# Optimization experiments

Measured on AMD Instinct MI355X. Metric: run time of the kernel, lower is better.

## Reference

```python
import jax, jax.numpy as jnp
import numpy as np

V, D, C, L, F = 32000, 1024, 2048, 6, 4096
B, S = 2, 2048


def _layer_norm(x, w, b, eps=1e-5):
    mu = jnp.mean(x, axis=-1, keepdims=True)
    var = jnp.mean(jnp.square(x - mu), axis=-1, keepdims=True)
    return (x - mu) * jax.lax.rsqrt(var + eps) * w + b


def setup_inputs() -> dict:
    key = jax.random.key(0)
    ks = jax.random.split(key, 16)
    s = 0.02
    inp = {
        "tokens": jax.random.randint(ks[0], (B, S), 0, V),
        "embed_table": jax.random.normal(ks[1], (V, D), jnp.float32) * s,
        "pos_table": jax.random.normal(ks[2], (C, D), jnp.float32) * s,
        # stacked per-layer params [L, ...]
        "ln1_w": jnp.ones((L, D), jnp.float32),
        "ln1_b": jnp.zeros((L, D), jnp.float32),
        "qkv_w": jax.random.normal(ks[3], (L, 3 * D, D), jnp.float32) * s,
        "qkv_b": jnp.zeros((L, 3 * D), jnp.float32),
        "ln2_w": jnp.ones((L, D), jnp.float32),
        "ln2_b": jnp.zeros((L, D), jnp.float32),
        "ffa_w": jax.random.normal(ks[4], (L, F, D), jnp.float32) * s,
        "ffa_b": jnp.zeros((L, F), jnp.float32),
        "ffb_w": jax.random.normal(ks[5], (L, D, F), jnp.float32) * s,
        "ffb_b": jnp.zeros((L, D), jnp.float32),
        "out_w": jax.random.normal(ks[6], (V, D), jnp.float32) * s,
    }
    return inp


def _forward(tokens, embed_table, pos_table, ln1_w, ln1_b, qkv_w, qkv_b,
             ln2_w, ln2_b, ffa_w, ffa_b, ffb_w, ffb_b, out_w):
    Sx = tokens.shape[1]
    h = embed_table[tokens] + pos_table[:Sx][None, :, :]  # [B,S,D]
    causal = jnp.triu(jnp.ones((Sx, Sx), bool), k=1)       # True = masked
    scale = jnp.float32(D) ** 0.5

    def block(h, p):
        l1w, l1b, qw, qb, l2w, l2b, aw, ab, bw, bb = p
        a = _layer_norm(h, l1w, l1b)
        qkv = jnp.einsum('bsd,ed->bse', a, qw) + qb       # [B,S,3D]
        q, k, v = jnp.split(qkv, 3, axis=-1)
        scores = jnp.einsum('bsd,btd->bst', q, k)          # [B,S,S]
        scores = jnp.where(causal[None], -jnp.inf, scores)
        attn = jax.nn.softmax(scores / scale, axis=-1)
        h = h + jnp.einsum('bst,btd->bsd', attn, v)
        f = _layer_norm(h, l2w, l2b)
        f = jax.nn.relu(jnp.einsum('bsd,fd->bsf', f, aw) + ab)
        h = h + jnp.einsum('bsf,df->bsd', f, bw) + bb
        return h, None

    params = (ln1_w, ln1_b, qkv_w, qkv_b, ln2_w, ln2_b, ffa_w, ffa_b, ffb_w, ffb_b)
    h, _ = jax.lax.scan(block, h, params)
    # OutputLayer applies only the Linear (output_norm is defined but unused)
    return jnp.einsum('bsd,vd->bsv', h, out_w)


def reference(tokens, embed_table, pos_table, ln1_w, ln1_b, qkv_w, qkv_b,
              ln2_w, ln2_b, ffa_w, ffa_b, ffb_w, ffb_b, out_w):
    return _forward(tokens, embed_table, pos_table, ln1_w, ln1_b, qkv_w, qkv_b,
                    ln2_w, ln2_b, ffa_w, ffa_b, ffb_w, ffb_b, out_w)
```

## Files before the change

kernel.cpp:

```cpp
#include <hip/hip_runtime.h>

#define Dm 1024
#define Sm 2048
#define Bm 2
#define Lm 6
#define Fm 4096
#define Vm 32000
#define MT (Bm*Sm)

typedef unsigned short u16;
typedef unsigned int   u32;
typedef __attribute__((ext_vector_type(8))) short bf16x8;
typedef __attribute__((ext_vector_type(4))) float f32x4;

__device__ __forceinline__ u16 f2bf(float f) {
  u32 u = __float_as_uint(f);
  u += 0x7fffu + ((u >> 16) & 1u);
  return (u16)(u >> 16);
}
__device__ __forceinline__ u32 pack2(float a, float b) {
  return (u32)f2bf(a) | ((u32)f2bf(b) << 16);
}
__device__ __forceinline__ void gload16(const void* g, void* l) {
  __builtin_amdgcn_global_load_lds(
      (const __attribute__((address_space(1))) void*)g,
      (__attribute__((address_space(3))) void*)l, 16, 0, 0);
}

__global__ __launch_bounds__(256) void embed_kernel(
    const int* __restrict__ tok, const float* __restrict__ emb,
    const float* __restrict__ pos, float* __restrict__ h)
{
  int i  = blockIdx.x * 256 + threadIdx.x;
  int d  = (i & (Dm/4 - 1)) * 4;
  int bs = i >> 8;
  int s  = bs & (Sm - 1);
  int t  = tok[bs];
  float4 e = *(const float4*)(emb + (size_t)t * Dm + d);
  float4 p = *(const float4*)(pos + (size_t)s * Dm + d);
  float4 r; r.x = e.x + p.x; r.y = e.y + p.y; r.z = e.z + p.z; r.w = e.w + p.w;
  *(float4*)(h + (size_t)bs * Dm + d) = r;
}

__global__ __launch_bounds__(256) void ln_kernel(
    const float* __restrict__ x, const float* __restrict__ w,
    const float* __restrict__ b, u16* __restrict__ o)
{
  __shared__ float red[8];
  int row = blockIdx.x, tid = threadIdx.x;
  const float* xr = x + (size_t)row * Dm;
  float4 v = *(const float4*)(xr + tid * 4);
  float s1 = v.x + v.y + v.z + v.w;
  float s2 = v.x*v.x + v.y*v.y + v.z*v.z + v.w*v.w;
  #pragma unroll
  for (int off = 32; off; off >>= 1) {
    s1 += __shfl_down(s1, off, 64);
    s2 += __shfl_down(s2, off, 64);
  }
  int lane = tid & 63, wv = tid >> 6;
  if (!lane) { red[wv] = s1; red[4 + wv] = s2; }
  __syncthreads();
  s1 = red[0] + red[1] + red[2] + red[3];
  s2 = red[4] + red[5] + red[6] + red[7];
  float mu = s1 * (1.f / Dm);
  float rs = rsqrtf(s2 * (1.f / Dm) - mu * mu + 1e-5f);
  float4 wv4 = *(const float4*)(w + tid * 4);
  float4 bv4 = *(const float4*)(b + tid * 4);
  uint2 pk;
  pk.x = pack2((v.x - mu) * rs * wv4.x + bv4.x, (v.y - mu) * rs * wv4.y + bv4.y);
  pk.y = pack2((v.z - mu) * rs * wv4.z + bv4.z, (v.w - mu) * rs * wv4.w + bv4.w);
  *(uint2*)(o + (size_t)row * Dm + tid * 4) = pk;
}

__global__ __launch_bounds__(256) void softmax_kernel(
    const float* __restrict__ sc, u16* __restrict__ at)
{
  __shared__ float red[8];
  int gr = blockIdx.x;
  int s  = gr & (Sm - 1);
  const float* x = sc + (size_t)gr * Sm;
  u16* o = at + (size_t)gr * Sm;
  int tid = threadIdx.x;
  float4 v0 = *(const float4*)(x + tid * 8);
  float4 v1 = *(const float4*)(x + tid * 8 + 4);
  float vals[8] = {v0.x, v0.y, v0.z, v0.w, v1.x, v1.y, v1.z, v1.w};
  float mx = -1e30f;
  #pragma unroll
  for (int j = 0; j < 8; ++j) {
    int t = tid * 8 + j;
    vals[j] = (t <= s) ? vals[j] * 0.03125f : -1e30f;
    mx = fmaxf(mx, vals[j]);
  }
  #pragma unroll
  for (int off = 32; off; off >>= 1) mx = fmaxf(mx, __shfl_down(mx, off, 64));
  int lane = tid & 63, wv = tid >> 6;
  if (!lane) red[wv] = mx;
  __syncthreads();
  mx = fmaxf(fmaxf(red[0], red[1]), fmaxf(red[2], red[3]));
  __syncthreads();
  float e[8], sm = 0.f;
  #pragma unroll
  for (int j = 0; j < 8; ++j) {
    int t = tid * 8 + j;
    e[j] = (t <= s) ? __expf(vals[j] - mx) : 0.f;
    sm += e[j];
  }
  #pragma unroll
  for (int off = 32; off; off >>= 1) sm += __shfl_down(sm, off, 64);
  if (!lane) red[wv] = sm;
  __syncthreads();
  sm = red[0] + red[1] + red[2] + red[3];
  float inv = 1.f / sm;
  uint4 p;
  p.x = pack2(e[0]*inv, e[1]*inv); p.y = pack2(e[2]*inv, e[3]*inv);
  p.z = pack2(e[4]*inv, e[5]*inv); p.w = pack2(e[6]*inv, e[7]*inv);
  *(uint4*)(o + tid * 8) = p;
}

__global__ __launch_bounds__(256) void cvt8_kernel(
    const float* __restrict__ x, u16* __restrict__ o)
{
  size_t i = ((size_t)blockIdx.x * 256 + threadIdx.x) * 8;
  float4 v0 = *(const float4*)(x + i);
  float4 v1 = *(const float4*)(x + i + 4);
  uint4 p; p.x = pack2(v0.x, v0.y); p.y = pack2(v0.z, v0.w);
  p.z = pack2(v1.x, v1.y); p.w = pack2(v1.z, v1.w);
  *(uint4*)(o + i) = p;
}

__global__ __launch_bounds__(256) void cvtw_kernel(
    const float* __restrict__ qw, const float* __restrict__ aw,
    const float* __restrict__ bw, u16* __restrict__ o)
{
  int b = blockIdx.x;
  const float* src; u16* dst; int idx;
  if (b < 1536)      { src = qw; dst = o;                     idx = b; }
  else if (b < 3584) { src = aw; dst = o + 3*Dm*Dm;           idx = b - 1536; }
  else               { src = bw; dst = o + 3*Dm*Dm + Fm*Dm;   idx = b - 3584; }
  size_t i = ((size_t)idx * 256 + threadIdx.x) * 8;
  float4 v0 = *(const float4*)(src + i);
  float4 v1 = *(const float4*)(src + i + 4);
  uint4 p; p.x = pack2(v0.x, v0.y); p.y = pack2(v0.z, v0.w);
  p.z = pack2(v1.x, v1.y); p.w = pack2(v1.z, v1.w);
  *(uint4*)(dst + i) = p;
}

__global__ __launch_bounds__(256) void vtr_kernel(
    const u16* __restrict__ v, u16* __restrict__ vT)
{
  __shared__ u16 t[64][64];
  int b = blockIdx.z;
  int s0 = blockIdx.x * 64, d0 = blockIdx.y * 64;
  const u16* src = v + ((size_t)b * Sm + s0) * (3 * Dm) + d0;
  int tid = threadIdx.x;
  int rr = tid >> 3, cc = (tid & 7) * 8;
  #pragma unroll
  for (int it = 0; it < 2; ++it) {
    int r = rr + it * 32;
    uint4 x = *(const uint4*)(src + (size_t)r * (3 * Dm) + cc);
    *(uint4*)&t[r][cc ^ (((r >> 3) & 7) << 3)] = x;
  }
  __syncthreads();
  u16* dst = vT + ((size_t)b * Dm + d0) * Sm + s0;
  #pragma unroll
  for (int it = 0; it < 2; ++it) {
    int d = rr + it * 32;
    u16 tmp[8];
    #pragma unroll
    for (int j = 0; j < 8; ++j) {
      int r = cc + j;
      tmp[j] = t[r][d ^ (((r >> 3) & 7) << 3)];
    }
    *(uint4*)(dst + (size_t)d * Sm + cc) = *(uint4*)tmp;
  }
}

enum { EPI_F32 = 0, EPI_BF16 = 1, EPI_RELU_BF16 = 2, EPI_RES = 3 };

__global__ __launch_bounds__(256, 2)
void gemm_kernel(const u16* __restrict__ A, const u16* __restrict__ B,
                 float* __restrict__ outF, u16* __restrict__ outB,
                 const float* __restrict__ bias, const float* __restrict__ resid,
                 int N, int K, int lda, int ldb,
                 long sA, long sB, long sO, long sR,
                 int mshift, int epi, int swz)
{
  __shared__ __align__(16) short As[128 * 64];
  __shared__ __align__(16) short Bs[128 * 64];

  const int z = blockIdx.z;
  int bid = blockIdx.x;
  if (swz) { int cpx = gridDim.x >> 3; bid = (bid & 7) * cpx + (bid >> 3); }
  const int m0 = (bid & ((1 << mshift) - 1)) << 7;
  const int n0 = (bid >> mshift) << 7;

  const u16* Az = A + (size_t)z * sA;
  const u16* Bz = B + (size_t)z * sB;

  const int tid = threadIdx.x;
  const int l   = tid & 63;
  const int w   = tid >> 6;
  const int sub = l >> 3;
  const int colb = ((l & 7) ^ sub) << 4;
  const int row0 = w * 32 + sub;

  const char* gA = (const char*)(Az + (size_t)(m0 + row0) * lda) + colb;
  const char* gB = (const char*)(Bz + (size_t)(n0 + row0) * ldb) + colb;
  const size_t stepA = (size_t)8 * lda * 2;
  const size_t stepB = (size_t)8 * ldb * 2;
  char* lA = (char*)As + w * 4096;
  char* lB = (char*)Bs + w * 4096;

  const int wm   = (w >> 1) * 64;
  const int wn   = (w & 1) * 64;
  const int lrow = l & 15;
  const int kgrp = l >> 4;

  f32x4 acc[4][4];
  #pragma unroll
  for (int i = 0; i < 4; ++i)
    #pragma unroll
    for (int j = 0; j < 4; ++j)
      acc[i][j] = (f32x4){0.f, 0.f, 0.f, 0.f};

  for (int k0 = 0; k0 < K; k0 += 64) {
    __syncthreads();
    const char* ga = gA + (size_t)k0 * 2;
    const char* gb = gB + (size_t)k0 * 2;
    #pragma unroll
    for (int c = 0; c < 4; ++c) {
      gload16(ga + c * stepA, lA + c * 1024);
      gload16(gb + c * stepB, lB + c * 1024);
    }
    __syncthreads();
    #pragma unroll
    for (int kk = 0; kk < 2; ++kk) {
      bf16x8 af[4], bf_[4];
      #pragma unroll
      for (int i = 0; i < 4; ++i) {
        int ar = wm + i * 16 + lrow;
        af[i]  = *(const bf16x8*)((const char*)As + ar * 128 +
                                  ((kk * 64 + kgrp * 16) ^ ((ar & 7) << 4)));
        int br = wn + i * 16 + lrow;
        bf_[i] = *(const bf16x8*)((const char*)Bs + br * 128 +
                                  ((kk * 64 + kgrp * 16) ^ ((br & 7) << 4)));
      }
      #pragma unroll
      for (int i = 0; i < 4; ++i)
        #pragma unroll
        for (int j = 0; j < 4; ++j)
          acc[i][j] = __builtin_amdgcn_mfma_f32_16x16x32_bf16(af[i], bf_[j], acc[i][j], 0, 0, 0);
    }
  }

  #pragma unroll
  for (int i = 0; i < 4; ++i) {
    #pragma unroll
    for (int j = 0; j < 4; ++j) {
      #pragma unroll
      for (int r = 0; r < 4; ++r) {
        int m = m0 + wm + i * 16 + kgrp * 4 + r;
        int n = n0 + wn + j * 16 + lrow;
        float v = acc[i][j][r];
        if (bias) v += bias[n];
        if (epi == EPI_F32) {
          outF[(size_t)z * sO + (size_t)m * N + n] = v;
        } else if (epi == EPI_BF16) {
          outB[(size_t)m * N + n] = f2bf(v);
        } else if (epi == EPI_RELU_BF16) {
          outB[(size_t)m * N + n] = f2bf(fmaxf(v, 0.f));
        } else {
          float* o = outF + (size_t)z * sO;
          const float* rsd = resid + (size_t)z * sR;
          o[(size_t)m * N + n] = rsd[(size_t)m * N + n] + v;
        }
      }
    }
  }
}

extern "C" void kernel_launch(void* const* d_in, const int* in_sizes, int n_in,
                              void* d_out, int out_size, void* d_ws, size_t ws_size,
                              hipStream_t stream)
{
  const int*   tok  = (const int*)d_in[0];
  const float* emb  = (const float*)d_in[1];
  const float* pos  = (const float*)d_in[2];
  const float* ln1w = (const float*)d_in[3];
  const float* ln1b = (const float*)d_in[4];
  const float* qkvw = (const float*)d_in[5];
  const float* qkvb = (const float*)d_in[6];
  const float* ln2w = (const float*)d_in[7];
  const float* ln2b = (const float*)d_in[8];
  const float* ffaw = (const float*)d_in[9];
  const float* ffab = (const float*)d_in[10];
  const float* ffbw = (const float*)d_in[11];
  const float* ffbb = (const float*)d_in[12];
  const float* outw = (const float*)d_in[13];
  float* out = (float*)d_out;

  char* p = (char*)d_ws;
  float* h      = (float*)p;  p += (size_t)MT * Dm * 4;
  u16*   a      = (u16*)p;    p += (size_t)MT * Dm * 2;
  u16*   hb     = (u16*)p;    p += (size_t)MT * Dm * 2;
  u16*   qkv    = (u16*)p;    p += (size_t)MT * 3 * Dm * 2;
  u16*   vT     = (u16*)p;    p += (size_t)Bm * Dm * Sm * 2;
  float* scores = (float*)p;  p += (size_t)Bm * Sm * Sm * 4;
  u16*   attn   = (u16*)p;    p += (size_t)Bm * Sm * Sm * 2;
  u16*   f      = (u16*)p;    p += (size_t)MT * Fm * 2;
  u16*   wlb    = (u16*)p;    p += (size_t)(3*Dm*Dm + Fm*Dm + Dm*Fm) * 2;
  u16*   owb    = qkv;

  embed_kernel<<<MT * Dm / 1024, 256, 0, stream>>>(tok, emb, pos, h);

  for (int l = 0; l < Lm; ++l) {
    cvtw_kernel<<<5632, 256, 0, stream>>>(
        qkvw + (size_t)l * 3 * Dm * Dm, ffaw + (size_t)l * Fm * Dm,
        ffbw + (size_t)l * Dm * Fm, wlb);
    ln_kernel<<<MT, 256, 0, stream>>>(h, ln1w + l * Dm, ln1b + l * Dm, a);
    gemm_kernel<<<dim3(768, 1, 1), 256, 0, stream>>>(
        a, wlb, nullptr, qkv, qkvb + l * 3 * Dm, nullptr,
        3 * Dm, Dm, Dm, Dm, 0, 0, 0, 0, 5, EPI_BF16, 1);
    gemm_kernel<<<dim3(256, 1, Bm), 256, 0, stream>>>(
        qkv, qkv + Dm, scores, nullptr, nullptr, nullptr,
        Sm, Dm, 3 * Dm, 3 * Dm, (long)Sm * 3 * Dm, (long)Sm * 3 * Dm,
        (long)Sm * Sm, 0, 4, EPI_F32, 0);
    softmax_kernel<<<Bm * Sm, 256, 0, stream>>>(scores, attn);
    vtr_kernel<<<dim3(32, 16, Bm), 256, 0, stream>>>(qkv + 2 * Dm, vT);
    gemm_kernel<<<dim3(128, 1, Bm), 256, 0, stream>>>(
        attn, vT, h, nullptr, nullptr, h,
        Dm, Sm, Sm, Sm, (long)Sm * Sm, (long)Dm * Sm,
        (long)Sm * Dm, (long)Sm * Dm, 4, EPI_RES, 0);
    ln_kernel<<<MT, 256, 0, stream>>>(h, ln2w + l * Dm, ln2b + l * Dm, a);
    gemm_kernel<<<dim3(1024, 1, 1), 256, 0, stream>>>(
        a, wlb + 3 * Dm * Dm, nullptr, f, ffab + l * Fm, nullptr,
        Fm, Dm, Dm, Dm, 0, 0, 0, 0, 5, EPI_RELU_BF16, 1);
    gemm_kernel<<<dim3(256, 1, 1), 256, 0, stream>>>(
        f, wlb + 3 * Dm * Dm + Fm * Dm, h, nullptr, ffbb + l * Dm, h,
        Dm, Fm, Fm, Fm, 0, 0, 0, 0, 5, EPI_RES, 1);
  }

  cvt8_kernel<<<MT * Dm / 2048, 256, 0, stream>>>(h, hb);
  cvt8_kernel<<<Vm * Dm / 2048, 256, 0, stream>>>(outw, owb);
  gemm_kernel<<<dim3(8000, 1, 1), 256, 0, stream>>>(
      hb, owb, out, nullptr, nullptr, nullptr,
      Vm, Dm, Dm, Dm, 0, 0, 0, 0, 5, EPI_F32, 1);
}
```

Before: 2.245 ms.

## Add 256x256 double-buffered 8-wave GEMM for QKV, FFN-up and output projection

Introduces a new GEMM kernel with 256x256 output tiles, 512 threads and 128KB of dynamic LDS. It double-buffers K-tiles using direct global-to-LDS loads, interleaves the staging loads with MFMA phases, and raises wave priority during the matrix math. The QKV, FFN-up and vocabulary-projection GEMMs move to it, and the final fp32 output uses nontemporal stores. Larger tiles cut global traffic per FLOP, but the heavy LDS use limits occupancy, and some grids (192 blocks) may underfill the CUs.

```diff
diff --git a/kernel.cpp b/kernel.cpp
--- a/kernel.cpp
+++ b/kernel.cpp
@@ -175,7 +175,7 @@
   }
 }
 
-enum { EPI_F32 = 0, EPI_BF16 = 1, EPI_RELU_BF16 = 2, EPI_RES = 3 };
+enum { EPI_F32 = 0, EPI_BF16 = 1, EPI_RELU_BF16 = 2, EPI_RES = 3, EPI_F32NT = 4 };
 
 __global__ __launch_bounds__(256, 2)
 void gemm_kernel(const u16* __restrict__ A, const u16* __restrict__ B,
@@ -279,6 +279,143 @@
   }
 }
 
+#define BAR_IN()  { __builtin_amdgcn_s_barrier(); \
+                    asm volatile("s_waitcnt lgkmcnt(0)" ::: "memory"); \
+                    __builtin_amdgcn_sched_barrier(0); \
+                    __builtin_amdgcn_s_setprio(1); }
+#define BAR_OUT() { __builtin_amdgcn_s_setprio(0); \
+                    __builtin_amdgcn_sched_barrier(0); \
+                    __builtin_amdgcn_s_barrier(); }
+
+__global__ __launch_bounds__(512, 2)
+void gemm256_kernel(const u16* __restrict__ A, const u16* __restrict__ B,
+                    float* __restrict__ outF, u16* __restrict__ outB,
+                    const float* __restrict__ bias,
+                    int N, int K, int mshift, int epi)
+{
+  extern __shared__ char lds[];
+
+  int bid = blockIdx.x;
+  { int cpx = gridDim.x >> 3; bid = (bid & 7) * cpx + (bid >> 3); }
+  const int m0 = (bid & ((1 << mshift) - 1)) << 8;
+  const int n0 = (bid >> mshift) << 8;
+
+  const int tid = threadIdx.x;
+  const int l = tid & 63, w = tid >> 6;
+  const int wr = w >> 2, wc = w & 3;
+  const int lrow = l & 15, kgrp = l >> 4;
+  const int wrbase = wr * 128, wcbase = wc * 64;
+  const int srow = (w << 3) + (l >> 3);
+  const int scol = ((l & 7) ^ (l >> 3)) << 3;
+  const int nt = K >> 6;
+
+  f32x4 acc[8][4];
+  #pragma unroll
+  for (int i = 0; i < 8; ++i)
+    #pragma unroll
+    for (int j = 0; j < 4; ++j)
+      acc[i][j] = (f32x4){0.f, 0.f, 0.f, 0.f};
+
+  auto STG = [&](int slot, const u16* gb, int grow0, int kel) {
+    const u16* g = gb + (size_t)(grow0 + srow) * K + kel + scol;
+    gload16(g, lds + slot + w * 1024);
+    gload16(g + (size_t)64 * K, lds + slot + 8192 + w * 1024);
+  };
+
+  STG(0,              A, m0,       0);
+  STG(16384,          A, m0 + 128, 0);
+  STG(32768,          B, n0,       0);
+  STG(49152,          B, n0 + 128, 0);
+  STG(65536 + 32768,  B, n0,       64);
+  STG(65536 + 49152,  B, n0 + 128, 64);
+  asm volatile("s_waitcnt vmcnt(4)" ::: "memory");
+  __builtin_amdgcn_s_barrier();
+
+  bf16x8 af[4][2], bfr[4][2];
+
+  #define RDA(base, q) { _Pragma("unroll") \
+    for (int f2 = 0; f2 < 4; ++f2) { _Pragma("unroll") \
+      for (int kk = 0; kk < 2; ++kk) { \
+        int row = wrbase + (q) * 64 + f2 * 16 + lrow; \
+        af[f2][kk] = *(const bf16x8*)((base) + row * 128 + \
+                       ((kk * 64 + kgrp * 16) ^ ((row & 7) << 4))); } } }
+  #define RDB(base, h) { _Pragma("unroll") \
+    for (int j2 = 0; j2 < 2; ++j2) { _Pragma("unroll") \
+      for (int kk = 0; kk < 2; ++kk) { \
+        int row = wcbase + ((h) * 2 + j2) * 16 + lrow; \
+        bfr[(h) * 2 + j2][kk] = *(const bf16x8*)((base) + row * 128 + \
+                       ((kk * 64 + kgrp * 16) ^ ((row & 7) << 4))); } } }
+  #define MM(fi0, fj0) { _Pragma("unroll") \
+    for (int f2 = 0; f2 < 4; ++f2) { _Pragma("unroll") \
+      for (int j2 = 0; j2 < 2; ++j2) { _Pragma("unroll") \
+        for (int kk = 0; kk < 2; ++kk) \
+          acc[(fi0) + f2][(fj0) + j2] = __builtin_amdgcn_mfma_f32_16x16x32_bf16( \
+              af[f2][kk], bfr[(fj0) + j2][kk], acc[(fi0) + f2][(fj0) + j2], 0, 0, 0); } } }
+
+  for (int i = 0; i < (nt >> 1); ++i) {
+    const int ta = 2 * i, tb = 2 * i + 1;
+    const int kA  = tb << 6;
+    const int kN0 = (ta + 2 < nt ? ta + 2 : ta + 2 - nt) << 6;
+    const int kN1 = (tb + 2 < nt ? tb + 2 : tb + 2 - nt) << 6;
+    const char* cA = lds;
+    const char* cB = lds + 32768;
+    RDA(cA, 0); RDB(cB, 0);
+    STG(65536, A, m0, kA);
+    BAR_IN(); MM(0, 0); BAR_OUT();
+    RDB(cB, 1);
+    STG(65536 + 16384, A, m0 + 128, kA);
+    BAR_IN(); MM(0, 2); BAR_OUT();
+    RDA(cA, 1);
+    STG(32768, B, n0, kN0);
+    BAR_IN(); MM(4, 0); BAR_OUT();
+    STG(49152, B, n0 + 128, kN0);
+    BAR_IN(); MM(4, 2);
+    __builtin_amdgcn_s_setprio(0);
+    __builtin_amdgcn_sched_barrier(0);
+    asm volatile("s_waitcnt vmcnt(4)" ::: "memory");
+    __builtin_amdgcn_s_barrier();
+    cA = lds + 65536; cB = lds + 65536 + 32768;
+    RDA(cA, 0); RDB(cB, 0);
+    STG(0, A, m0, kN0);
+    BAR_IN(); MM(0, 0); BAR_OUT();
+    RDB(cB, 1);
+    STG(16384, A, m0 + 128, kN0);
+    BAR_IN(); MM(0, 2); BAR_OUT();
+    RDA(cA, 1);
+    STG(65536 + 32768, B, n0, kN1);
+    BAR_IN(); MM(4, 0); BAR_OUT();
+    STG(65536 + 49152, B, n0 + 128, kN1);
+    BAR_IN(); MM(4, 2);
+    __builtin_amdgcn_s_setprio(0);
+    __builtin_amdgcn_sched_barrier(0);
+    asm volatile("s_waitcnt vmcnt(4)" ::: "memory");
+    __builtin_amdgcn_s_barrier();
+  }
+
+  #pragma unroll
+  for (int fi = 0; fi < 8; ++fi) {
+    #pragma unroll
+    for (int fj = 0; fj < 4; ++fj) {
+      #pragma unroll
+      for (int r = 0; r < 4; ++r) {
+        int m = m0 + wrbase + fi * 16 + kgrp * 4 + r;
+        int n = n0 + wcbase + fj * 16 + lrow;
+        float v = acc[fi][fj][r];
+        if (bias) v += bias[n];
+        if (epi == EPI_F32) {
+          outF[(size_t)m * N + n] = v;
+        } else if (epi == EPI_F32NT) {
+          __builtin_nontemporal_store(v, outF + (size_t)m * N + n);
+        } else if (epi == EPI_BF16) {
+          outB[(size_t)m * N + n] = f2bf(v);
+        } else {
+          outB[(size_t)m * N + n] = f2bf(fmaxf(v, 0.f));
+        }
+      }
+    }
+  }
+}
+
 extern "C" void kernel_launch(void* const* d_in, const int* in_sizes, int n_in,
                               void* d_out, int out_size, void* d_ws, size_t ws_size,
                               hipStream_t stream)
@@ -299,6 +436,11 @@
   const float* outw = (const float*)d_in[13];
   float* out = (float*)d_out;
 
+  static bool attr_set = false;
+  hipFuncSetAttribute((const void*)gemm256_kernel,
+                      hipFuncAttributeMaxDynamicSharedMemorySize, 131072);
+  (void)attr_set;
+
   char* p = (char*)d_ws;
   float* h      = (float*)p;  p += (size_t)MT * Dm * 4;
   u16*   a      = (u16*)p;    p += (size_t)MT * Dm * 2;
@@ -318,9 +460,8 @@
         qkvw + (size_t)l * 3 * Dm * Dm, ffaw + (size_t)l * Fm * Dm,
         ffbw + (size_t)l * Dm * Fm, wlb);
     ln_kernel<<<MT, 256, 0, stream>>>(h, ln1w + l * Dm, ln1b + l * Dm, a);
-    gemm_kernel<<<dim3(768, 1, 1), 256, 0, stream>>>(
-        a, wlb, nullptr, qkv, qkvb + l * 3 * Dm, nullptr,
-        3 * Dm, Dm, Dm, Dm, 0, 0, 0, 0, 5, EPI_BF16, 1);
+    gemm256_kernel<<<dim3(192), 512, 131072, stream>>>(
+        a, wlb, nullptr, qkv, qkvb + l * 3 * Dm, 3 * Dm, Dm, 4, EPI_BF16);
     gemm_kernel<<<dim3(256, 1, Bm), 256, 0, stream>>>(
         qkv, qkv + Dm, scores, nullptr, nullptr, nullptr,
         Sm, Dm, 3 * Dm, 3 * Dm, (long)Sm * 3 * Dm, (long)Sm * 3 * Dm,
@@ -332,9 +473,8 @@
         Dm, Sm, Sm, Sm, (long)Sm * Sm, (long)Dm * Sm,
         (long)Sm * Dm, (long)Sm * Dm, 4, EPI_RES, 0);
     ln_kernel<<<MT, 256, 0, stream>>>(h, ln2w + l * Dm, ln2b + l * Dm, a);
-    gemm_kernel<<<dim3(1024, 1, 1), 256, 0, stream>>>(
-        a, wlb + 3 * Dm * Dm, nullptr, f, ffab + l * Fm, nullptr,
-        Fm, Dm, Dm, Dm, 0, 0, 0, 0, 5, EPI_RELU_BF16, 1);
+    gemm256_kernel<<<dim3(256), 512, 131072, stream>>>(
+        a, wlb + 3 * Dm * Dm, nullptr, f, ffab + l * Fm, Fm, Dm, 4, EPI_RELU_BF16);
     gemm_kernel<<<dim3(256, 1, 1), 256, 0, stream>>>(
         f, wlb + 3 * Dm * Dm + Fm * Dm, h, nullptr, ffbb + l * Dm, h,
         Dm, Fm, Fm, Fm, 0, 0, 0, 0, 5, EPI_RES, 1);
@@ -342,7 +482,6 @@
 
   cvt8_kernel<<<MT * Dm / 2048, 256, 0, stream>>>(h, hb);
   cvt8_kernel<<<Vm * Dm / 2048, 256, 0, stream>>>(outw, owb);
-  gemm_kernel<<<dim3(8000, 1, 1), 256, 0, stream>>>(
-      hb, owb, out, nullptr, nullptr, nullptr,
-      Vm, Dm, Dm, Dm, 0, 0, 0, 0, 5, EPI_F32, 1);
-}
+  gemm256_kernel<<<dim3(2000), 512, 131072, stream>>>(
+      hb, owb, out, nullptr, nullptr, Vm, Dm, 4, EPI_F32NT);
+}
```

Measured after the change: 2.301 ms. +2.5%, slower.

## Skip causal-masked attention tiles, double-buffer GEMM LDS, use nontemporal logit stores

Applied to the files above, without the earlier changes.

The GEMM kernel gains a causal mode. In the QK^T GEMM, tiles lying entirely above the diagonal return early. In the attention-times-V GEMM, the K loop stops at the diagonal, since softmax zeroes probabilities past it. The K loop now double-buffers the A/B tiles in LDS, so the next tile's global-to-LDS load overlaps the current tile's MFMAs; this doubles shared memory per block. The final vocabulary projection writes its fp32 logits with nontemporal stores to limit cache pollution. Skipped score tiles stay uninitialised, so correctness depends on softmax masking them.

```diff
diff --git a/kernel.cpp b/kernel.cpp
--- a/kernel.cpp
+++ b/kernel.cpp
@@ -175,7 +175,7 @@
   }
 }
 
-enum { EPI_F32 = 0, EPI_BF16 = 1, EPI_RELU_BF16 = 2, EPI_RES = 3 };
+enum { EPI_F32 = 0, EPI_BF16 = 1, EPI_RELU_BF16 = 2, EPI_RES = 3, EPI_F32NT = 4 };
 
 __global__ __launch_bounds__(256, 2)
 void gemm_kernel(const u16* __restrict__ A, const u16* __restrict__ B,
@@ -183,16 +183,20 @@
                  const float* __restrict__ bias, const float* __restrict__ resid,
                  int N, int K, int lda, int ldb,
                  long sA, long sB, long sO, long sR,
-                 int mshift, int epi, int swz)
-{
-  __shared__ __align__(16) short As[128 * 64];
-  __shared__ __align__(16) short Bs[128 * 64];
+                 int mshift, int epi, int swz, int cmode)
+{
+  __shared__ __align__(16) short As[2][128 * 64];
+  __shared__ __align__(16) short Bs[2][128 * 64];
 
   const int z = blockIdx.z;
   int bid = blockIdx.x;
   if (swz) { int cpx = gridDim.x >> 3; bid = (bid & 7) * cpx + (bid >> 3); }
   const int m0 = (bid & ((1 << mshift) - 1)) << 7;
   const int n0 = (bid >> mshift) << 7;
+
+  if (cmode == 1 && n0 > m0) return;
+  const int keff = (cmode == 2) ? min(K, m0 + 128) : K;
+  const int nt = keff >> 6;
 
   const u16* Az = A + (size_t)z * sA;
   const u16* Bz = B + (size_t)z * sB;
@@ -208,8 +212,6 @@
   const char* gB = (const char*)(Bz + (size_t)(n0 + row0) * ldb) + colb;
   const size_t stepA = (size_t)8 * lda * 2;
   const size_t stepB = (size_t)8 * ldb * 2;
-  char* lA = (char*)As + w * 4096;
-  char* lB = (char*)Bs + w * 4096;
 
   const int wm   = (w >> 1) * 64;
   const int wn   = (w & 1) * 64;
@@ -223,26 +225,36 @@
     for (int j = 0; j < 4; ++j)
       acc[i][j] = (f32x4){0.f, 0.f, 0.f, 0.f};
 
-  for (int k0 = 0; k0 < K; k0 += 64) {
-    __syncthreads();
-    const char* ga = gA + (size_t)k0 * 2;
-    const char* gb = gB + (size_t)k0 * 2;
+  auto STAGE = [&](int buf, int t) {
+    const char* ga = gA + (size_t)t * 128;
+    const char* gb = gB + (size_t)t * 128;
+    char* la = (char*)As[buf] + w * 4096;
+    char* lb = (char*)Bs[buf] + w * 4096;
     #pragma unroll
     for (int c = 0; c < 4; ++c) {
-      gload16(ga + c * stepA, lA + c * 1024);
-      gload16(gb + c * stepB, lB + c * 1024);
+      gload16(ga + c * stepA, la + c * 1024);
+      gload16(gb + c * stepB, lb + c * 1024);
     }
-    __syncthreads();
+  };
+
+  STAGE(0, 0);
+  __syncthreads();
+
+  for (int t = 0; t < nt; ++t) {
+    const int cur = t & 1;
+    if (t + 1 < nt) STAGE(cur ^ 1, t + 1);
+    const char* bA = (const char*)As[cur];
+    const char* bB = (const char*)Bs[cur];
     #pragma unroll
     for (int kk = 0; kk < 2; ++kk) {
       bf16x8 af[4], bf_[4];
       #pragma unroll
       for (int i = 0; i < 4; ++i) {
         int ar = wm + i * 16 + lrow;
-        af[i]  = *(const bf16x8*)((const char*)As + ar * 128 +
+        af[i]  = *(const bf16x8*)(bA + ar * 128 +
                                   ((kk * 64 + kgrp * 16) ^ ((ar & 7) << 4)));
         int br = wn + i * 16 + lrow;
-        bf_[i] = *(const bf16x8*)((const char*)Bs + br * 128 +
+        bf_[i] = *(const bf16x8*)(bB + br * 128 +
                                   ((kk * 64 + kgrp * 16) ^ ((br & 7) << 4)));
       }
       #pragma unroll
@@ -251,6 +263,7 @@
         for (int j = 0; j < 4; ++j)
           acc[i][j] = __builtin_amdgcn_mfma_f32_16x16x32_bf16(af[i], bf_[j], acc[i][j], 0, 0, 0);
     }
+    __syncthreads();
   }
 
   #pragma unroll
@@ -265,6 +278,8 @@
         if (bias) v += bias[n];
         if (epi == EPI_F32) {
           outF[(size_t)z * sO + (size_t)m * N + n] = v;
+        } else if (epi == EPI_F32NT) {
+          __builtin_nontemporal_store(v, outF + (size_t)m * N + n);
         } else if (epi == EPI_BF16) {
           outB[(size_t)m * N + n] = f2bf(v);
         } else if (epi == EPI_RELU_BF16) {
@@ -320,29 +335,29 @@
     ln_kernel<<<MT, 256, 0, stream>>>(h, ln1w + l * Dm, ln1b + l * Dm, a);
     gemm_kernel<<<dim3(768, 1, 1), 256, 0, stream>>>(
         a, wlb, nullptr, qkv, qkvb + l * 3 * Dm, nullptr,
-        3 * Dm, Dm, Dm, Dm, 0, 0, 0, 0, 5, EPI_BF16, 1);
+        3 * Dm, Dm, Dm, Dm, 0, 0, 0, 0, 5, EPI_BF16, 1, 0);
     gemm_kernel<<<dim3(256, 1, Bm), 256, 0, stream>>>(
         qkv, qkv + Dm, scores, nullptr, nullptr, nullptr,
         Sm, Dm, 3 * Dm, 3 * Dm, (long)Sm * 3 * Dm, (long)Sm * 3 * Dm,
-        (long)Sm * Sm, 0, 4, EPI_F32, 0);
+        (long)Sm * Sm, 0, 4, EPI_F32, 0, 1);
     softmax_kernel<<<Bm * Sm, 256, 0, stream>>>(scores, attn);
     vtr_kernel<<<dim3(32, 16, Bm), 256, 0, stream>>>(qkv + 2 * Dm, vT);
     gemm_kernel<<<dim3(128, 1, Bm), 256, 0, stream>>>(
         attn, vT, h, nullptr, nullptr, h,
         Dm, Sm, Sm, Sm, (long)Sm * Sm, (long)Dm * Sm,
-        (long)Sm * Dm, (long)Sm * Dm, 4, EPI_RES, 0);
+        (long)Sm * Dm, (long)Sm * Dm, 4, EPI_RES, 0, 2);
     ln_kernel<<<MT, 256, 0, stream>>>(h, ln2w + l * Dm, ln2b + l * Dm, a);
     gemm_kernel<<<dim3(1024, 1, 1), 256, 0, stream>>>(
         a, wlb + 3 * Dm * Dm, nullptr, f, ffab + l * Fm, nullptr,
-        Fm, Dm, Dm, Dm, 0, 0, 0, 0, 5, EPI_RELU_BF16, 1);
+        Fm, Dm, Dm, Dm, 0, 0, 0, 0, 5, EPI_RELU_BF16, 1, 0);
     gemm_kernel<<<dim3(256, 1, 1), 256, 0, stream>>>(
         f, wlb + 3 * Dm * Dm + Fm * Dm, h, nullptr, ffbb + l * Dm, h,
-        Dm, Fm, Fm, Fm, 0, 0, 0, 0, 5, EPI_RES, 1);
+        Dm, Fm, Fm, Fm, 0, 0, 0, 0, 5, EPI_RES, 1, 0);
   }
 
   cvt8_kernel<<<MT * Dm / 2048, 256, 0, stream>>>(h, hb);
   cvt8_kernel<<<Vm * Dm / 2048, 256, 0, stream>>>(outw, owb);
   gemm_kernel<<<dim3(8000, 1, 1), 256, 0, stream>>>(
       hb, owb, out, nullptr, nullptr, nullptr,
-      Vm, Dm, Dm, Dm, 0, 0, 0, 0, 5, EPI_F32, 1);
-}
+      Vm, Dm, Dm, Dm, 0, 0, 0, 0, 5, EPI_F32NT, 1, 0);
+}
```

After: 2.480 ms. +10.5%, slower.
